# Optimization experiments

Hardware: AMD Instinct MI355X
Metric: run time of the kernel (lower is better)

## Reference

```python
import jax, jax.numpy as jnp
import numpy as np

N_TOKENS, E, H = 20000, 128, 512
B, T, L = 128, 512, 8


def setup_inputs() -> dict:
    key = jax.random.key(0)
    ks = jax.random.split(key, 9)
    s = 0.02
    return {
        "tokens": jax.random.randint(ks[0], (B, T, L), 0, N_TOKENS),
        "values": jax.random.uniform(ks[1], (B, T, L), dtype=jnp.float32),
        "emb": jax.random.normal(ks[2], (N_TOKENS, E), dtype=jnp.float32) * s,
        "W_ih": jax.random.normal(ks[3], (4 * H, E), dtype=jnp.float32) * s,
        "W_hh": jax.random.normal(ks[4], (4 * H, H), dtype=jnp.float32) * s,
        "b_ih": jnp.zeros((4 * H,), jnp.float32),
        "b_hh": jnp.zeros((4 * H,), jnp.float32),
        "W_out": jax.random.normal(ks[5], (1, H), dtype=jnp.float32) * s,
        "b_out": jnp.zeros((1,), jnp.float32),
    }


def reference(tokens, values, emb, W_ih, W_hh, b_ih, b_hh, W_out, b_out):
    # EmbedTimeseriesW: value-weighted sum of token embeddings per time bin
    e = emb[tokens]                                  # [B,T,L,E]
    x = jnp.einsum('btle,btl->bte', e, values)       # [B,T,E]
    x = jax.nn.relu(x)                               # ReLU (dropout p=0 -> identity)

    xT = jnp.swapaxes(x, 0, 1)                       # [T,B,E]
    b = b_ih + b_hh

    def step(carry, xt):
        h, c = carry
        gates = xt @ W_ih.T + h @ W_hh.T + b         # [B,4H]
        i, f, g, o = jnp.split(gates, 4, axis=-1)    # torch LSTM gate order
        c = jax.nn.sigmoid(f) * c + jax.nn.sigmoid(i) * jnp.tanh(g)
        h = jax.nn.sigmoid(o) * jnp.tanh(c)
        return (h, c), h

    h0 = jnp.zeros((x.shape[0], W_hh.shape[1]), x.dtype)
    (_, _), hs = jax.lax.scan(step, (h0, h0), xT)    # hs: [T,B,H]

    out = jnp.swapaxes(hs, 0, 1) @ W_out.T + b_out   # [B,T,1]
    return out.squeeze(-1)                           # [B,T]
```

## Files before the change

### kernel.cpp

```cpp
#include <hip/hip_runtime.h>
#include <hip/hip_bf16.h>

#define B_   128
#define T_   512
#define L_   8
#define E_   128
#define H_   512

#define BG_   4
#define WPG_  16
#define JW_   32
#define HU64_ (B_ * H_ / 4)
#define GSTR  132

typedef __attribute__((ext_vector_type(8))) short s8v;
typedef __attribute__((ext_vector_type(4))) float f4v;
typedef unsigned long long u64;

__device__ __forceinline__ float bf16u_to_f(unsigned short s) {
  union { unsigned u; float f; } c; c.u = ((unsigned)s) << 16; return c.f;
}
__device__ __forceinline__ u64 llc_load8(const void* p) {
  return __hip_atomic_load((const u64*)p, __ATOMIC_RELAXED, __HIP_MEMORY_SCOPE_AGENT);
}
__device__ __forceinline__ void llc_store8(void* p, u64 v) {
  __hip_atomic_store((u64*)p, v, __ATOMIC_RELAXED, __HIP_MEMORY_SCOPE_AGENT);
}
__device__ __forceinline__ unsigned llc_load4(const unsigned* p) {
  return __hip_atomic_load(p, __ATOMIC_RELAXED, __HIP_MEMORY_SCOPE_AGENT);
}
__device__ __forceinline__ void llc_store4(unsigned* p, unsigned v) {
  __hip_atomic_store(p, v, __ATOMIC_RELAXED, __HIP_MEMORY_SCOPE_AGENT);
}
__device__ __forceinline__ float sigf(float x) {
  return __builtin_amdgcn_rcpf(1.f + __expf(-x));
}
__device__ __forceinline__ float tanh_f(float x) {
  return 1.f - 2.f * __builtin_amdgcn_rcpf(1.f + __expf(2.f * x));
}

__device__ __forceinline__ void wait_flags64(const unsigned* flags, unsigned tgt) {
  const unsigned* p = flags + (threadIdx.x & 63);
  while (!__all((int)(llc_load4(p) >= tgt))) { }
}

__global__ void embed_kernel(const int* __restrict__ tokens,
                             const float* __restrict__ values,
                             const float* __restrict__ emb,
                             __hip_bfloat16* __restrict__ x_bf) {
  int idx = blockIdx.x * blockDim.x + threadIdx.x;
  int e  = idx & (E_ - 1);
  int bt = idx >> 7;
  int b  = bt >> 9;
  int t  = bt & (T_ - 1);
  const int*   tok = tokens + (size_t)bt * L_;
  const float* val = values + (size_t)bt * L_;
  float acc = 0.f;
#pragma unroll
  for (int l = 0; l < L_; ++l) acc += emb[(size_t)tok[l] * E_ + e] * val[l];
  acc = fmaxf(acc, 0.f);
  x_bf[((size_t)t * B_ + b) * E_ + e] = __float2bfloat16(acc);
}

__device__ __forceinline__ void out_dot_lds(const u64* __restrict__ h_lds,
                                            int t, int bg,
                                            const float* __restrict__ wout_s,
                                            float bout, float* __restrict__ out) {
  const int um = threadIdx.x >> 3;
  const int uj = threadIdx.x & 7;
  const u64* row = h_lds + (size_t)um * 128;
  const float* wr = wout_s + uj * 64;
  float p = 0.f;
#pragma unroll
  for (int j = 0; j < 8; ++j) {
    int pc = ((uj * 8 + j) ^ (um & 7)) * 2;
    u64 qa = row[pc], qb = row[pc + 1];
    p += bf16u_to_f((unsigned short)(qa      )) * wr[j * 8 + 0];
    p += bf16u_to_f((unsigned short)(qa >> 16)) * wr[j * 8 + 1];
    p += bf16u_to_f((unsigned short)(qa >> 32)) * wr[j * 8 + 2];
    p += bf16u_to_f((unsigned short)(qa >> 48)) * wr[j * 8 + 3];
    p += bf16u_to_f((unsigned short)(qb      )) * wr[j * 8 + 4];
    p += bf16u_to_f((unsigned short)(qb >> 16)) * wr[j * 8 + 5];
    p += bf16u_to_f((unsigned short)(qb >> 32)) * wr[j * 8 + 6];
    p += bf16u_to_f((unsigned short)(qb >> 48)) * wr[j * 8 + 7];
  }
  p += __shfl_down(p, 4, 8);
  p += __shfl_down(p, 2, 8);
  p += __shfl_down(p, 1, 8);
  if (uj == 0) out[(size_t)(bg * 32 + um) * T_ + t] = p + bout;
}

__device__ __forceinline__ void out_dot_glb(const u64* __restrict__ h,
                                            int t, int bg,
                                            const float* __restrict__ wout_s,
                                            float bout, float* __restrict__ out) {
  const int um = threadIdx.x >> 3;
  const int uj = threadIdx.x & 7;
  const int b  = bg * 32 + um;
  const u64* hr = h + (size_t)b * 128 + uj * 16;
  const float* wr = wout_s + uj * 64;
  float p = 0.f;
#pragma unroll
  for (int kk = 0; kk < 16; ++kk) {
    u64 q = llc_load8(hr + kk);
    p += bf16u_to_f((unsigned short)(q      )) * wr[kk * 4 + 0];
    p += bf16u_to_f((unsigned short)(q >> 16)) * wr[kk * 4 + 1];
    p += bf16u_to_f((unsigned short)(q >> 32)) * wr[kk * 4 + 2];
    p += bf16u_to_f((unsigned short)(q >> 48)) * wr[kk * 4 + 3];
  }
  p += __shfl_down(p, 4, 8);
  p += __shfl_down(p, 2, 8);
  p += __shfl_down(p, 1, 8);
  if (uj == 0) out[(size_t)b * T_ + t] = p + bout;
}

__global__ void __launch_bounds__(256, 1)
lstm_kernel(const float* __restrict__ W_ih, const float* __restrict__ W_hh,
            const float* __restrict__ b_ih, const float* __restrict__ b_hh,
            const float* __restrict__ W_out, const float* __restrict__ b_out,
            const __hip_bfloat16* __restrict__ x_bf,
            u64* __restrict__ h_base,
            float* __restrict__ out,
            unsigned* __restrict__ bars) {
  __shared__ __align__(16) u64   h_lds[32 * 128];
  __shared__ __align__(16) float gbuf[32][GSTR];
  __shared__ __align__(16) float bias_s[128];
  __shared__ float wout_s[H_];

  const int tid = threadIdx.x;
  const int wg  = blockIdx.x;
  const int bg  = wg >> 4;
  const int g   = wg & (WPG_ - 1);
  const int j0g = g * JW_;

  const int wv   = tid >> 6;
  const int lane = tid & 63;
  const int m16  = lane & 15;
  const int q    = lane >> 4;
  const int sw   = m16 & 7;

  s8v bfrag[2][20];
#pragma unroll
  for (int nt = 0; nt < 2; ++nt) {
    const int r = wv * H_ + j0g + nt * 16 + m16;
    const float* wih_r = W_ih + (size_t)r * E_;
    const float* whh_r = W_hh + (size_t)r * H_;
#pragma unroll
    for (int ks = 0; ks < 20; ++ks) {
      s8v v;
#pragma unroll
      for (int i = 0; i < 8; ++i) {
        int k = ks * 32 + q * 8 + i;
        float w = (k < E_) ? wih_r[k] : whh_r[k - E_];
        __hip_bfloat16 hb = __float2bfloat16(w);
        v[i] = *(short*)&hb;
      }
      bfrag[nt][ks] = v;
    }
  }
  if (tid < 128) {
    int gt = tid >> 5, jl = tid & 31;
    int r = gt * H_ + j0g + jl;
    bias_s[tid] = b_ih[r] + b_hh[r];
  }
  if (g == 0) for (int i = tid; i < H_; i += 256) wout_s[i] = W_out[i];

  const int um = tid >> 3;
  const int jb = (tid & 7) * 4;
  const int ub = bg * 32 + um;
  const int fc = tid & 7;
  float cst[4] = {0.f, 0.f, 0.f, 0.f};
  const float bout = b_out[0];
  unsigned* flags  = bars + bg * 64;
  unsigned* myflag = flags + (g << 2) + wv;

  int rp = 2, wp = 0;
  f4v acc[2][2];

  {
    const __hip_bfloat16* ax0 = x_bf + (size_t)(bg * 32 + m16) * E_ + q * 8;
    const __hip_bfloat16* ax1 = x_bf + (size_t)(bg * 32 + 16 + m16) * E_ + q * 8;
    f4v z = {0.f, 0.f, 0.f, 0.f};
    acc[0][0] = z; acc[0][1] = z; acc[1][0] = z; acc[1][1] = z;
#pragma unroll
    for (int ks = 0; ks < 4; ++ks) {
      s8v a0 = *(const s8v*)(ax0 + ks * 32);
      s8v a1 = *(const s8v*)(ax1 + ks * 32);
#pragma unroll
      for (int nt = 0; nt < 2; ++nt) {
        acc[0][nt] = __builtin_amdgcn_mfma_f32_16x16x32_bf16(a0, bfrag[nt][ks], acc[0][nt], 0, 0, 0);
        acc[1][nt] = __builtin_amdgcn_mfma_f32_16x16x32_bf16(a1, bfrag[nt][ks], acc[1][nt], 0, 0, 0);
      }
    }
  }
  __syncthreads();

  for (int t = 0; t < T_; ++t) {
    const u64* h_prev = h_base + (size_t)rp * HU64_;
    u64*       h_next = h_base + (size_t)wp * HU64_;

    wait_flags64(flags, (unsigned)t);

    {
      const u64* src = h_prev + (size_t)(bg * 32 + um) * 128;
      u64 v[16];
#pragma unroll
      for (int j = 0; j < 8; ++j) {
        int lc = fc + 8 * j;
        v[2 * j]     = llc_load8(src + lc * 2);
        v[2 * j + 1] = llc_load8(src + lc * 2 + 1);
      }
      u64* dst = h_lds + (size_t)um * 128;
#pragma unroll
      for (int j = 0; j < 8; ++j) {
        int pc = ((fc + 8 * j) ^ (um & 7)) * 2;
        dst[pc]     = v[2 * j];
        dst[pc + 1] = v[2 * j + 1];
      }
    }
    __syncthreads();

    {
      const u64* al0 = h_lds + (size_t)m16 * 128;
      const u64* al1 = h_lds + (size_t)(16 + m16) * 128;
#pragma unroll
      for (int ks4 = 0; ks4 < 16; ++ks4) {
        int pc = ((ks4 * 4 + q) ^ sw) * 2;
        s8v a0 = *(const s8v*)(al0 + pc);
        s8v a1 = *(const s8v*)(al1 + pc);
#pragma unroll
        for (int nt = 0; nt < 2; ++nt) {
          acc[0][nt] = __builtin_amdgcn_mfma_f32_16x16x32_bf16(a0, bfrag[nt][4 + ks4], acc[0][nt], 0, 0, 0);
          acc[1][nt] = __builtin_amdgcn_mfma_f32_16x16x32_bf16(a1, bfrag[nt][4 + ks4], acc[1][nt], 0, 0, 0);
        }
      }
    }

#pragma unroll
    for (int mt = 0; mt < 2; ++mt)
#pragma unroll
      for (int nt = 0; nt < 2; ++nt)
#pragma unroll
        for (int r = 0; r < 4; ++r)
          gbuf[mt * 16 + q * 4 + r][wv * 32 + nt * 16 + m16] = acc[mt][nt][r];
    __syncthreads();

    {
      const float* gr = &gbuf[0][0] + (size_t)um * GSTR;
      f4v vi = *(const f4v*)(gr + jb);
      f4v vf = *(const f4v*)(gr + 32 + jb);
      f4v vg = *(const f4v*)(gr + 64 + jb);
      f4v vo = *(const f4v*)(gr + 96 + jb);
      f4v bi = *(const f4v*)(bias_s + jb);
      f4v bf = *(const f4v*)(bias_s + 32 + jb);
      f4v bgc = *(const f4v*)(bias_s + 64 + jb);
      f4v bo = *(const f4v*)(bias_s + 96 + jb);
      u64 packed = 0;
#pragma unroll
      for (int qq = 0; qq < 4; ++qq) {
        float si = sigf(vi[qq] + bi[qq]);
        float sf = sigf(vf[qq] + bf[qq]);
        float tg = tanh_f(vg[qq] + bgc[qq]);
        float so = sigf(vo[qq] + bo[qq]);
        cst[qq] = sf * cst[qq] + si * tg;
        float h = so * tanh_f(cst[qq]);
        __hip_bfloat16 hb = __float2bfloat16(h);
        packed |= (u64)(*(unsigned short*)&hb) << (16 * qq);
      }
      llc_store8(h_next + (size_t)ub * 128 + ((j0g + jb) >> 2), packed);
    }
    asm volatile("s_waitcnt vmcnt(0)" ::: "memory");
    if (lane == 0) llc_store4(myflag, (unsigned)(t + 1));

    if (g == 0 && t > 0)
      out_dot_lds(h_lds, t - 1, bg, wout_s, bout, out);

    if (t + 1 < T_) {
      const __hip_bfloat16* xt = x_bf + (size_t)(t + 1) * B_ * E_;
      const __hip_bfloat16* ax0 = xt + (size_t)(bg * 32 + m16) * E_ + q * 8;
      const __hip_bfloat16* ax1 = xt + (size_t)(bg * 32 + 16 + m16) * E_ + q * 8;
      f4v z = {0.f, 0.f, 0.f, 0.f};
      acc[0][0] = z; acc[0][1] = z; acc[1][0] = z; acc[1][1] = z;
#pragma unroll
      for (int ks = 0; ks < 4; ++ks) {
        s8v a0 = *(const s8v*)(ax0 + ks * 32);
        s8v a1 = *(const s8v*)(ax1 + ks * 32);
#pragma unroll
        for (int nt = 0; nt < 2; ++nt) {
          acc[0][nt] = __builtin_amdgcn_mfma_f32_16x16x32_bf16(a0, bfrag[nt][ks], acc[0][nt], 0, 0, 0);
          acc[1][nt] = __builtin_amdgcn_mfma_f32_16x16x32_bf16(a1, bfrag[nt][ks], acc[1][nt], 0, 0, 0);
        }
      }
    }

    __syncthreads();

    rp = wp; wp = (wp == 2) ? 0 : wp + 1;
  }

  wait_flags64(flags, (unsigned)T_);
  if (g == 0)
    out_dot_glb(h_base + (size_t)rp * HU64_, T_ - 1, bg, wout_s, bout, out);
}

extern "C" void kernel_launch(void* const* d_in, const int* in_sizes, int n_in,
                              void* d_out, int out_size, void* d_ws, size_t ws_size,
                              hipStream_t stream) {
  const int*   tokens = (const int*)d_in[0];
  const float* values = (const float*)d_in[1];
  const float* emb    = (const float*)d_in[2];
  const float* W_ih   = (const float*)d_in[3];
  const float* W_hh   = (const float*)d_in[4];
  const float* b_ih   = (const float*)d_in[5];
  const float* b_hh   = (const float*)d_in[6];
  const float* W_out  = (const float*)d_in[7];
  const float* b_out  = (const float*)d_in[8];
  float* out = (float*)d_out;

  char* ws = (char*)d_ws;
  __hip_bfloat16* x_bf = (__hip_bfloat16*)ws;
  u64* h_base = (u64*)(ws + (size_t)T_ * B_ * E_ * 2);
  unsigned* bars = (unsigned*)(ws + (size_t)T_ * B_ * E_ * 2
                                  + (size_t)3 * HU64_ * sizeof(u64));

  hipMemsetAsync(h_base, 0, (size_t)3 * HU64_ * sizeof(u64), stream);
  hipMemsetAsync(bars, 0, (size_t)BG_ * 64 * sizeof(unsigned), stream);

  embed_kernel<<<(B_ * T_ * E_) / 256, 256, 0, stream>>>(tokens, values, emb, x_bf);

  lstm_kernel<<<dim3(BG_ * WPG_), dim3(256), 0, stream>>>(
      W_ih, W_hh, b_ih, b_hh, W_out, b_out, x_bf, h_base, out, bars);
}
```

Baseline: 2.337 ms.

## Replace flag barrier with per-element step tags embedded in hidden-state words

Removes the separate flag array and the vmcnt wait plus flag store. Each bf16 hidden value is now paired with a 16-bit timestep tag inside its 32-bit word. Readers spin on the h data itself until every tag matches the expected step. This drops one round-trip of flag polling per step, but doubles the size of the h exchange buffer and the global load and store traffic. The 16-bit tag stays valid because T=512.

```diff
diff --git a/kernel.cpp b/kernel.cpp
--- a/kernel.cpp
+++ b/kernel.cpp
@@ -10,7 +10,7 @@
 #define BG_   4
 #define WPG_  16
 #define JW_   32
-#define HU64_ (B_ * H_ / 4)
+#define SLOTQ (B_ * H_ / 2)
 #define GSTR  132
 
 typedef __attribute__((ext_vector_type(8))) short s8v;
@@ -26,23 +26,16 @@
 __device__ __forceinline__ void llc_store8(void* p, u64 v) {
   __hip_atomic_store((u64*)p, v, __ATOMIC_RELAXED, __HIP_MEMORY_SCOPE_AGENT);
 }
-__device__ __forceinline__ unsigned llc_load4(const unsigned* p) {
-  return __hip_atomic_load(p, __ATOMIC_RELAXED, __HIP_MEMORY_SCOPE_AGENT);
-}
-__device__ __forceinline__ void llc_store4(unsigned* p, unsigned v) {
-  __hip_atomic_store(p, v, __ATOMIC_RELAXED, __HIP_MEMORY_SCOPE_AGENT);
-}
 __device__ __forceinline__ float sigf(float x) {
   return __builtin_amdgcn_rcpf(1.f + __expf(-x));
 }
 __device__ __forceinline__ float tanh_f(float x) {
   return 1.f - 2.f * __builtin_amdgcn_rcpf(1.f + __expf(2.f * x));
 }
-
-__device__ __forceinline__ void wait_flags64(const unsigned* flags, unsigned tgt) {
-  const unsigned* p = flags + (threadIdx.x & 63);
-  while (!__all((int)(llc_load4(p) >= tgt))) { }
-}
+__device__ __forceinline__ unsigned pk(u64 w) {
+  return (unsigned)((w >> 16) & 0xFFFFu) | (unsigned)((w >> 48) << 16);
+}
+#define TAGMASK 0x0000FFFF0000FFFFULL
 
 __global__ void embed_kernel(const int* __restrict__ tokens,
                              const float* __restrict__ values,
@@ -90,23 +83,30 @@
   if (uj == 0) out[(size_t)(bg * 32 + um) * T_ + t] = p + bout;
 }
 
-__device__ __forceinline__ void out_dot_glb(const u64* __restrict__ h,
-                                            int t, int bg,
-                                            const float* __restrict__ wout_s,
-                                            float bout, float* __restrict__ out) {
+__device__ __forceinline__ void out_dot_glb_tagged(const u64* __restrict__ slot,
+                                                   int t, int bg, unsigned tag,
+                                                   const float* __restrict__ wout_s,
+                                                   float bout, float* __restrict__ out) {
   const int um = threadIdx.x >> 3;
   const int uj = threadIdx.x & 7;
   const int b  = bg * 32 + um;
-  const u64* hr = h + (size_t)b * 128 + uj * 16;
+  const u64* hr = slot + (size_t)b * 256 + uj * 32;
+  const u64 tagpair = (u64)tag | ((u64)tag << 32);
+  u64 w[32];
+  for (;;) {
+#pragma unroll
+    for (int i = 0; i < 32; ++i) w[i] = llc_load8(hr + i);
+    u64 bad = 0;
+#pragma unroll
+    for (int i = 0; i < 32; ++i) bad |= (w[i] & TAGMASK) ^ tagpair;
+    if (bad == 0) break;
+  }
   const float* wr = wout_s + uj * 64;
   float p = 0.f;
 #pragma unroll
-  for (int kk = 0; kk < 16; ++kk) {
-    u64 q = llc_load8(hr + kk);
-    p += bf16u_to_f((unsigned short)(q      )) * wr[kk * 4 + 0];
-    p += bf16u_to_f((unsigned short)(q >> 16)) * wr[kk * 4 + 1];
-    p += bf16u_to_f((unsigned short)(q >> 32)) * wr[kk * 4 + 2];
-    p += bf16u_to_f((unsigned short)(q >> 48)) * wr[kk * 4 + 3];
+  for (int i = 0; i < 32; ++i) {
+    p += bf16u_to_f((unsigned short)(w[i] >> 16)) * wr[2 * i];
+    p += bf16u_to_f((unsigned short)(w[i] >> 48)) * wr[2 * i + 1];
   }
   p += __shfl_down(p, 4, 8);
   p += __shfl_down(p, 2, 8);
@@ -120,8 +120,7 @@
             const float* __restrict__ W_out, const float* __restrict__ b_out,
             const __hip_bfloat16* __restrict__ x_bf,
             u64* __restrict__ h_base,
-            float* __restrict__ out,
-            unsigned* __restrict__ bars) {
+            float* __restrict__ out) {
   __shared__ __align__(16) u64   h_lds[32 * 128];
   __shared__ __align__(16) float gbuf[32][GSTR];
   __shared__ __align__(16) float bias_s[128];
@@ -171,8 +170,6 @@
   const int fc = tid & 7;
   float cst[4] = {0.f, 0.f, 0.f, 0.f};
   const float bout = b_out[0];
-  unsigned* flags  = bars + bg * 64;
-  unsigned* myflag = flags + (g << 2) + wv;
 
   int rp = 2, wp = 0;
   f4v acc[2][2];
@@ -196,26 +193,33 @@
   __syncthreads();
 
   for (int t = 0; t < T_; ++t) {
-    const u64* h_prev = h_base + (size_t)rp * HU64_;
-    u64*       h_next = h_base + (size_t)wp * HU64_;
-
-    wait_flags64(flags, (unsigned)t);
+    const u64* h_prev = h_base + (size_t)rp * SLOTQ;
+    u64*       h_next = h_base + (size_t)wp * SLOTQ;
 
     {
-      const u64* src = h_prev + (size_t)(bg * 32 + um) * 128;
-      u64 v[16];
-#pragma unroll
-      for (int j = 0; j < 8; ++j) {
-        int lc = fc + 8 * j;
-        v[2 * j]     = llc_load8(src + lc * 2);
-        v[2 * j + 1] = llc_load8(src + lc * 2 + 1);
+      const u64* src = h_prev + (size_t)(bg * 32 + um) * 256;
+      const u64 tagpair = (u64)(unsigned)t | ((u64)(unsigned)t << 32);
+      u64 w[32];
+      for (;;) {
+#pragma unroll
+        for (int j = 0; j < 8; ++j) {
+          int cb = (fc + 8 * j) * 4;
+          w[4 * j]     = llc_load8(src + cb);
+          w[4 * j + 1] = llc_load8(src + cb + 1);
+          w[4 * j + 2] = llc_load8(src + cb + 2);
+          w[4 * j + 3] = llc_load8(src + cb + 3);
+        }
+        u64 bad = 0;
+#pragma unroll
+        for (int i = 0; i < 32; ++i) bad |= (w[i] & TAGMASK) ^ tagpair;
+        if (bad == 0) break;
       }
       u64* dst = h_lds + (size_t)um * 128;
 #pragma unroll
       for (int j = 0; j < 8; ++j) {
         int pc = ((fc + 8 * j) ^ (um & 7)) * 2;
-        dst[pc]     = v[2 * j];
-        dst[pc + 1] = v[2 * j + 1];
+        dst[pc]     = (u64)pk(w[4 * j])     | ((u64)pk(w[4 * j + 1]) << 32);
+        dst[pc + 1] = (u64)pk(w[4 * j + 2]) | ((u64)pk(w[4 * j + 3]) << 32);
       }
     }
     __syncthreads();
@@ -255,7 +259,8 @@
       f4v bf = *(const f4v*)(bias_s + 32 + jb);
       f4v bgc = *(const f4v*)(bias_s + 64 + jb);
       f4v bo = *(const f4v*)(bias_s + 96 + jb);
-      u64 packed = 0;
+      const u64 tagp = (u64)(unsigned)(t + 1);
+      unsigned short hb[4];
 #pragma unroll
       for (int qq = 0; qq < 4; ++qq) {
         float si = sigf(vi[qq] + bi[qq]);
@@ -264,13 +269,15 @@
         float so = sigf(vo[qq] + bo[qq]);
         cst[qq] = sf * cst[qq] + si * tg;
         float h = so * tanh_f(cst[qq]);
-        __hip_bfloat16 hb = __float2bfloat16(h);
-        packed |= (u64)(*(unsigned short*)&hb) << (16 * qq);
-      }
-      llc_store8(h_next + (size_t)ub * 128 + ((j0g + jb) >> 2), packed);
-    }
-    asm volatile("s_waitcnt vmcnt(0)" ::: "memory");
-    if (lane == 0) llc_store4(myflag, (unsigned)(t + 1));
+        __hip_bfloat16 hx = __float2bfloat16(h);
+        hb[qq] = *(unsigned short*)&hx;
+      }
+      u64 s0 = tagp | ((u64)hb[0] << 16) | (tagp << 32) | ((u64)hb[1] << 48);
+      u64 s1 = tagp | ((u64)hb[2] << 16) | (tagp << 32) | ((u64)hb[3] << 48);
+      u64* dstp = h_next + (size_t)ub * 256 + ((j0g + jb) >> 1);
+      llc_store8(dstp, s0);
+      llc_store8(dstp + 1, s1);
+    }
 
     if (g == 0 && t > 0)
       out_dot_lds(h_lds, t - 1, bg, wout_s, bout, out);
@@ -298,9 +305,9 @@
     rp = wp; wp = (wp == 2) ? 0 : wp + 1;
   }
 
-  wait_flags64(flags, (unsigned)T_);
   if (g == 0)
-    out_dot_glb(h_base + (size_t)rp * HU64_, T_ - 1, bg, wout_s, bout, out);
+    out_dot_glb_tagged(h_base + (size_t)rp * SLOTQ, T_ - 1, bg, (unsigned)T_,
+                       wout_s, bout, out);
 }
 
 extern "C" void kernel_launch(void* const* d_in, const int* in_sizes, int n_in,
@@ -320,14 +327,11 @@
   char* ws = (char*)d_ws;
   __hip_bfloat16* x_bf = (__hip_bfloat16*)ws;
   u64* h_base = (u64*)(ws + (size_t)T_ * B_ * E_ * 2);
-  unsigned* bars = (unsigned*)(ws + (size_t)T_ * B_ * E_ * 2
-                                  + (size_t)3 * HU64_ * sizeof(u64));
-
-  hipMemsetAsync(h_base, 0, (size_t)3 * HU64_ * sizeof(u64), stream);
-  hipMemsetAsync(bars, 0, (size_t)BG_ * 64 * sizeof(unsigned), stream);
+
+  hipMemsetAsync(h_base, 0, (size_t)3 * SLOTQ * sizeof(u64), stream);
 
   embed_kernel<<<(B_ * T_ * E_) / 256, 256, 0, stream>>>(tokens, values, emb, x_bf);
 
   lstm_kernel<<<dim3(BG_ * WPG_), dim3(256), 0, stream>>>(
-      W_ih, W_hh, b_ih, b_hh, W_out, b_out, x_bf, h_base, out, bars);
-}
+      W_ih, W_hh, b_ih, b_hh, W_out, b_out, x_bf, h_base, out);
+}
```

Result: slower. 2.709 ms (+15.9%).
